# Kernel tuning notes

Measured on AMD Instinct MI355X. Metric: run time of the kernel, lower is better.

The kernel has to match this reference:

```python
import jax, jax.numpy as jnp
import numpy as np

B, H, S, D = 2, 16, 2048, 64

def setup_inputs() -> dict:
    key = jax.random.key(0)
    kq, kk, kv, km = jax.random.split(key, 4)
    Query = jax.random.normal(kq, (B, H, S, D), dtype=jnp.float32)
    Key = jax.random.normal(kk, (B, H, S, D), dtype=jnp.float32)
    Value = jax.random.normal(kv, (B, H, S, D), dtype=jnp.float32)
    attention_mask = jax.random.randint(km, (B, 1, S, S), 0, 2).astype(jnp.bool_)
    return {"Query": Query, "Key": Key, "Value": Value,
            "attention_mask": attention_mask, "dim_key": D}

def reference(Query, Key, Value, attention_mask, dim_key):
    # scores: [B,H,S,S]
    scale = 1.0 / np.sqrt(dim_key).astype(np.float32)
    scores = jnp.einsum('bhqd,bhkd->bhqk', Query, Key) * scale
    scores = jnp.where(attention_mask, jnp.float32(-1e9), scores)
    attention = jax.nn.softmax(scores, axis=-1)
    context = jnp.einsum('bhqk,bhkd->bhqd', attention, Value)
    return (context, attention)
```

## Files before the change

### kernel.cpp

```cpp
#include <hip/hip_runtime.h>
#include <hip/hip_bf16.h>


#define S_LEN 2048
#define D_DIM 64
#define LOG2E 1.44269504088896340736f

typedef __attribute__((ext_vector_type(8))) short bf16x8;
typedef __attribute__((ext_vector_type(4))) float f32x4;
typedef unsigned long long u64;

__device__ __forceinline__ unsigned int f2bs2(float x, float y) {
    union { __hip_bfloat162 h; unsigned int u; } u;
    u.h = __float22bfloat162_rn(make_float2(x, y));
    return u.u;
}
__device__ __forceinline__ short f2bs(float f) {
    union { __hip_bfloat16 h; short s; } u;
    u.h = __float2bfloat16(f);
    return u.s;
}
__device__ __forceinline__ bf16x8 cvt8(float4 a, float4 b) {
    union { bf16x8 v; unsigned int w[4]; } u;
    u.w[0] = f2bs2(a.x, a.y); u.w[1] = f2bs2(a.z, a.w);
    u.w[2] = f2bs2(b.x, b.y); u.w[3] = f2bs2(b.z, b.w);
    return u.v;
}

__device__ __forceinline__ void gl2lds16(const short* g, short* l) {
    __builtin_amdgcn_global_load_lds(
        (const __attribute__((address_space(1))) unsigned int*)g,
        (__attribute__((address_space(3))) unsigned int*)l, 16, 0, 0);
}

__global__ __launch_bounds__(256) void prep_kv(const float* __restrict__ K,
                                               const float* __restrict__ V,
                                               short* __restrict__ Kb,
                                               short* __restrict__ Vtb) {
    __shared__ short T[64 * 80];
    const int bh = blockIdx.x >> 5;
    const int kt = blockIdx.x & 31;
    const int k0 = kt * 64;
    const int t  = threadIdx.x;
    const int row = t >> 2;
    const int cq  = (t & 3) * 16;

    const size_t base = (size_t)bh * S_LEN * D_DIM;
    {
        const float* kp = K + base + (size_t)(k0 + row) * D_DIM + cq;
        float4 a = ((const float4*)kp)[0], b = ((const float4*)kp)[1],
               c = ((const float4*)kp)[2], d = ((const float4*)kp)[3];
        short* op = Kb + base + (size_t)(k0 + row) * D_DIM + cq;
        *(bf16x8*)op       = cvt8(a, b);
        *(bf16x8*)(op + 8) = cvt8(c, d);
    }
    {
        const float* vp = V + base + (size_t)(k0 + row) * D_DIM + cq;
        float4 a = ((const float4*)vp)[0], b = ((const float4*)vp)[1],
               c = ((const float4*)vp)[2], d = ((const float4*)vp)[3];
        float vv[16] = {a.x,a.y,a.z,a.w, b.x,b.y,b.z,b.w,
                        c.x,c.y,c.z,c.w, d.x,d.y,d.z,d.w};
        #pragma unroll
        for (int i = 0; i < 16; ++i)
            T[(cq + i) * 80 + row] = f2bs(vv[i]);
    }
    __syncthreads();
    {
        const int d  = t >> 2;
        const int kc = (t & 3) * 16;
        short* op = Vtb + (size_t)bh * D_DIM * S_LEN + (size_t)d * S_LEN + k0 + kc;
        *(bf16x8*)op       = *(const bf16x8*)&T[d * 80 + kc];
        *(bf16x8*)(op + 8) = *(const bf16x8*)&T[d * 80 + kc + 8];
    }
}

__global__ __launch_bounds__(256) void mask_pack(const int* __restrict__ M,
                                                 u64* __restrict__ Mp) {
    const int lane = threadIdx.x & 63;
    const int wid  = (blockIdx.x * 256 + threadIdx.x) >> 6;
    const int nwaves = gridDim.x * 4;
    const int nwords = 2 * S_LEN * (S_LEN / 64);
    for (int w = wid; w < nwords; w += nwaves) {
        int v = M[(size_t)w * 64 + lane];
        u64 bits = __ballot(v != 0);
        if (lane == 0) Mp[w] = bits;
    }
}

__global__ __launch_bounds__(256, 4) void sdpa_main(
    const float* __restrict__ Q, const short* __restrict__ Kb,
    const short* __restrict__ Vtb, const u64* __restrict__ Mp,
    float* __restrict__ Ctx, float* __restrict__ Attn)
{
    __shared__ short Kt[64 * 64];
    __shared__ short Vt[64 * 64];
    __shared__ short Pt[4 * 16 * 80];

    const int tid  = threadIdx.x;
    const int wave = tid >> 6;
    const int lane = tid & 63;
    const int quad = lane >> 4;
    const int l16  = lane & 15;

    const int bid = blockIdx.x;
    const int bh  = ((bid >> 8) << 3) | (bid & 7);
    const int qt  = (bid >> 3) & 31;
    const int b   = bh >> 4;
    const int qw  = qt * 64 + wave * 16;

    const size_t sd_off = (size_t)bh * S_LEN * D_DIM;
    const float* Qbh = Q + sd_off;
    const short* Kbh = Kb + sd_off;
    const short* Vbh = Vtb + (size_t)bh * D_DIM * S_LEN;
    float* Cbh = Ctx + sd_off;
    float* Abh = Attn + (size_t)bh * S_LEN * S_LEN;

    bf16x8 qfrag[2];
    {
        const int qrow = qw + l16;
        const float s = 0.125f * LOG2E;
        #pragma unroll
        for (int kc = 0; kc < 2; ++kc) {
            const float* qp = Qbh + (size_t)qrow * D_DIM + kc * 32 + quad * 8;
            float4 a = ((const float4*)qp)[0], c = ((const float4*)qp)[1];
            a.x*=s; a.y*=s; a.z*=s; a.w*=s; c.x*=s; c.y*=s; c.z*=s; c.w*=s;
            qfrag[kc] = cvt8(a, c);
        }
    }

    const int mrow0 = (b * S_LEN + qw + quad * 4) * (S_LEN / 64);

    float lacc[4] = {0.f, 0.f, 0.f, 0.f};
    for (int kt = 0; kt < 32; ++kt) {
        const int k0 = kt * 64;
        __syncthreads();
        #pragma unroll
        for (int rd = 0; rd < 2; ++rd) {
            const int m = tid + rd * 256;
            const int row = m >> 3, sc = m & 7, c = sc ^ (row & 7);
            gl2lds16(Kbh + (size_t)(k0 + row) * D_DIM + c * 8, &Kt[m * 8]);
        }
        __syncthreads();
        u64 mw[4];
        #pragma unroll
        for (int r = 0; r < 4; ++r) mw[r] = Mp[mrow0 + r * 32 + kt];
        #pragma unroll
        for (int cc = 0; cc < 4; ++cc) {
            const int keyl = cc * 16 + l16;
            f32x4 acc = {0.f, 0.f, 0.f, 0.f};
            #pragma unroll
            for (int kc = 0; kc < 2; ++kc) {
                bf16x8 bfr = *(const bf16x8*)&Kt[keyl * 64 + ((kc * 4 + quad) ^ (keyl & 7)) * 8];
                acc = __builtin_amdgcn_mfma_f32_16x16x32_bf16(qfrag[kc], bfr, acc, 0, 0, 0);
            }
            #pragma unroll
            for (int r = 0; r < 4; ++r) {
                float p = __builtin_amdgcn_exp2f(acc[r]);
                p = ((mw[r] >> keyl) & 1ull) ? 0.f : p;
                lacc[r] += p;
            }
        }
    }
    #pragma unroll
    for (int off = 1; off < 16; off <<= 1) {
        #pragma unroll
        for (int r = 0; r < 4; ++r) lacc[r] += __shfl_xor(lacc[r], off, 64);
    }
    float inv_l[4];
    #pragma unroll
    for (int r = 0; r < 4; ++r) inv_l[r] = 1.0f / lacc[r];

    f32x4 cacc[4];
    #pragma unroll
    for (int dc = 0; dc < 4; ++dc) cacc[dc] = (f32x4){0.f, 0.f, 0.f, 0.f};
    short* Pw = &Pt[wave * 16 * 80];

    for (int kt = 0; kt < 32; ++kt) {
        const int k0 = kt * 64;
        __syncthreads();
        #pragma unroll
        for (int rd = 0; rd < 2; ++rd) {
            const int m = tid + rd * 256;
            const int row = m >> 3, sc = m & 7, c = sc ^ (row & 7);
            gl2lds16(Kbh + (size_t)(k0 + row) * D_DIM + c * 8, &Kt[m * 8]);
            gl2lds16(Vbh + (size_t)row * S_LEN + k0 + c * 8, &Vt[m * 8]);
        }
        __syncthreads();
        u64 mw[4];
        #pragma unroll
        for (int r = 0; r < 4; ++r) mw[r] = Mp[mrow0 + r * 32 + kt];
        float* ap0 = Abh + (size_t)(qw + quad * 4) * S_LEN + k0;
        #pragma unroll
        for (int cc = 0; cc < 4; ++cc) {
            const int keyl = cc * 16 + l16;
            f32x4 acc = {0.f, 0.f, 0.f, 0.f};
            #pragma unroll
            for (int kc = 0; kc < 2; ++kc) {
                bf16x8 bfr = *(const bf16x8*)&Kt[keyl * 64 + ((kc * 4 + quad) ^ (keyl & 7)) * 8];
                acc = __builtin_amdgcn_mfma_f32_16x16x32_bf16(qfrag[kc], bfr, acc, 0, 0, 0);
            }
            #pragma unroll
            for (int r = 0; r < 4; ++r) {
                float p = __builtin_amdgcn_exp2f(acc[r]);
                p = ((mw[r] >> keyl) & 1ull) ? 0.f : p;
                __builtin_nontemporal_store(p * inv_l[r], ap0 + (size_t)r * S_LEN + keyl);
                Pw[(quad * 4 + r) * 80 + keyl] = f2bs(p);
            }
        }
        #pragma unroll
        for (int kc = 0; kc < 2; ++kc) {
            bf16x8 af = *(const bf16x8*)&Pw[l16 * 80 + kc * 32 + quad * 8];
            #pragma unroll
            for (int dc = 0; dc < 4; ++dc) {
                const int vrow = dc * 16 + l16;
                bf16x8 bfr = *(const bf16x8*)&Vt[vrow * 64 + ((kc * 4 + quad) ^ (vrow & 7)) * 8];
                cacc[dc] = __builtin_amdgcn_mfma_f32_16x16x32_bf16(af, bfr, cacc[dc], 0, 0, 0);
            }
        }
    }

    #pragma unroll
    for (int dc = 0; dc < 4; ++dc) {
        #pragma unroll
        for (int r = 0; r < 4; ++r) {
            Cbh[(size_t)(qw + quad * 4 + r) * D_DIM + dc * 16 + l16] =
                cacc[dc][r] * inv_l[r];
        }
    }
}

extern "C" void kernel_launch(void* const* d_in, const int* in_sizes, int n_in,
                              void* d_out, int out_size, void* d_ws, size_t ws_size,
                              hipStream_t stream) {
    const float* Q    = (const float*)d_in[0];
    const float* K    = (const float*)d_in[1];
    const float* V    = (const float*)d_in[2];
    const int*   Mask = (const int*)d_in[3];

    float* Ctx  = (float*)d_out;
    float* Attn = (float*)d_out + (size_t)2 * 16 * 2048 * 64;

    short* Kb  = (short*)d_ws;
    short* Vtb = (short*)((char*)d_ws + 8388608);
    u64*   Mp  = (u64*)((char*)d_ws + 16777216);

    prep_kv<<<dim3(1024), dim3(256), 0, stream>>>(K, V, Kb, Vtb);
    mask_pack<<<dim3(512), dim3(256), 0, stream>>>(Mask, Mp);
    sdpa_main<<<dim3(1024), dim3(256), 0, stream>>>(Q, Kb, Vtb, Mp, Ctx, Attn);
}
```

Before: 724.3 us.

## Load K/V MFMA fragments directly from global memory instead of staging through LDS

```diff
diff --git a/kernel.cpp b/kernel.cpp
--- a/kernel.cpp
+++ b/kernel.cpp
@@ -25,12 +25,6 @@
     u.w[0] = f2bs2(a.x, a.y); u.w[1] = f2bs2(a.z, a.w);
     u.w[2] = f2bs2(b.x, b.y); u.w[3] = f2bs2(b.z, b.w);
     return u.v;
-}
-
-__device__ __forceinline__ void gl2lds16(const short* g, short* l) {
-    __builtin_amdgcn_global_load_lds(
-        (const __attribute__((address_space(1))) unsigned int*)g,
-        (__attribute__((address_space(3))) unsigned int*)l, 16, 0, 0);
 }
 
 __global__ __launch_bounds__(256) void prep_kv(const float* __restrict__ K,
@@ -92,8 +86,6 @@
     const short* __restrict__ Vtb, const u64* __restrict__ Mp,
     float* __restrict__ Ctx, float* __restrict__ Attn)
 {
-    __shared__ short Kt[64 * 64];
-    __shared__ short Vt[64 * 64];
     __shared__ short Pt[4 * 16 * 80];
 
     const int tid  = threadIdx.x;
@@ -115,6 +107,9 @@
     float* Cbh = Ctx + sd_off;
     float* Abh = Attn + (size_t)bh * S_LEN * S_LEN;
 
+    const short* kfp = Kbh + (size_t)l16 * D_DIM + quad * 8;
+    const short* vfp = Vbh + (size_t)l16 * S_LEN + quad * 8;
+
     bf16x8 qfrag[2];
     {
         const int qrow = qw + l16;
@@ -128,31 +123,21 @@
         }
     }
 
-    const int mrow0 = (b * S_LEN + qw + quad * 4) * (S_LEN / 64);
+    const u64* mp = Mp + (size_t)(b * S_LEN + qw + quad * 4) * (S_LEN / 64);
 
     float lacc[4] = {0.f, 0.f, 0.f, 0.f};
     for (int kt = 0; kt < 32; ++kt) {
         const int k0 = kt * 64;
-        __syncthreads();
-        #pragma unroll
-        for (int rd = 0; rd < 2; ++rd) {
-            const int m = tid + rd * 256;
-            const int row = m >> 3, sc = m & 7, c = sc ^ (row & 7);
-            gl2lds16(Kbh + (size_t)(k0 + row) * D_DIM + c * 8, &Kt[m * 8]);
-        }
-        __syncthreads();
         u64 mw[4];
         #pragma unroll
-        for (int r = 0; r < 4; ++r) mw[r] = Mp[mrow0 + r * 32 + kt];
+        for (int r = 0; r < 4; ++r) mw[r] = mp[r * 32 + kt];
         #pragma unroll
         for (int cc = 0; cc < 4; ++cc) {
+            const short* kp = kfp + (size_t)(k0 + cc * 16) * D_DIM;
+            f32x4 acc = {0.f, 0.f, 0.f, 0.f};
+            acc = __builtin_amdgcn_mfma_f32_16x16x32_bf16(qfrag[0], *(const bf16x8*)kp,        acc, 0, 0, 0);
+            acc = __builtin_amdgcn_mfma_f32_16x16x32_bf16(qfrag[1], *(const bf16x8*)(kp + 32), acc, 0, 0, 0);
             const int keyl = cc * 16 + l16;
-            f32x4 acc = {0.f, 0.f, 0.f, 0.f};
-            #pragma unroll
-            for (int kc = 0; kc < 2; ++kc) {
-                bf16x8 bfr = *(const bf16x8*)&Kt[keyl * 64 + ((kc * 4 + quad) ^ (keyl & 7)) * 8];
-                acc = __builtin_amdgcn_mfma_f32_16x16x32_bf16(qfrag[kc], bfr, acc, 0, 0, 0);
-            }
             #pragma unroll
             for (int r = 0; r < 4; ++r) {
                 float p = __builtin_amdgcn_exp2f(acc[r]);
@@ -177,28 +162,27 @@
 
     for (int kt = 0; kt < 32; ++kt) {
         const int k0 = kt * 64;
-        __syncthreads();
-        #pragma unroll
-        for (int rd = 0; rd < 2; ++rd) {
-            const int m = tid + rd * 256;
-            const int row = m >> 3, sc = m & 7, c = sc ^ (row & 7);
-            gl2lds16(Kbh + (size_t)(k0 + row) * D_DIM + c * 8, &Kt[m * 8]);
-            gl2lds16(Vbh + (size_t)row * S_LEN + k0 + c * 8, &Vt[m * 8]);
-        }
-        __syncthreads();
         u64 mw[4];
         #pragma unroll
-        for (int r = 0; r < 4; ++r) mw[r] = Mp[mrow0 + r * 32 + kt];
+        for (int r = 0; r < 4; ++r) mw[r] = mp[r * 32 + kt];
+
+        bf16x8 vfr[2][4];
+        #pragma unroll
+        for (int kc = 0; kc < 2; ++kc) {
+            #pragma unroll
+            for (int dc = 0; dc < 4; ++dc) {
+                vfr[kc][dc] = *(const bf16x8*)(vfp + (size_t)dc * 16 * S_LEN + k0 + kc * 32);
+            }
+        }
+
         float* ap0 = Abh + (size_t)(qw + quad * 4) * S_LEN + k0;
         #pragma unroll
         for (int cc = 0; cc < 4; ++cc) {
+            const short* kp = kfp + (size_t)(k0 + cc * 16) * D_DIM;
+            f32x4 acc = {0.f, 0.f, 0.f, 0.f};
+            acc = __builtin_amdgcn_mfma_f32_16x16x32_bf16(qfrag[0], *(const bf16x8*)kp,        acc, 0, 0, 0);
+            acc = __builtin_amdgcn_mfma_f32_16x16x32_bf16(qfrag[1], *(const bf16x8*)(kp + 32), acc, 0, 0, 0);
             const int keyl = cc * 16 + l16;
-            f32x4 acc = {0.f, 0.f, 0.f, 0.f};
-            #pragma unroll
-            for (int kc = 0; kc < 2; ++kc) {
-                bf16x8 bfr = *(const bf16x8*)&Kt[keyl * 64 + ((kc * 4 + quad) ^ (keyl & 7)) * 8];
-                acc = __builtin_amdgcn_mfma_f32_16x16x32_bf16(qfrag[kc], bfr, acc, 0, 0, 0);
-            }
             #pragma unroll
             for (int r = 0; r < 4; ++r) {
                 float p = __builtin_amdgcn_exp2f(acc[r]);
@@ -212,9 +196,7 @@
             bf16x8 af = *(const bf16x8*)&Pw[l16 * 80 + kc * 32 + quad * 8];
             #pragma unroll
             for (int dc = 0; dc < 4; ++dc) {
-                const int vrow = dc * 16 + l16;
-                bf16x8 bfr = *(const bf16x8*)&Vt[vrow * 64 + ((kc * 4 + quad) ^ (vrow & 7)) * 8];
-                cacc[dc] = __builtin_amdgcn_mfma_f32_16x16x32_bf16(af, bfr, cacc[dc], 0, 0, 0);
+                cacc[dc] = __builtin_amdgcn_mfma_f32_16x16x32_bf16(af, vfr[kc][dc], cacc[dc], 0, 0, 0);
             }
         }
     }
```

Result: slower. 913.5 us (+26.1%).
